# Optimization experiments

Hardware: AMD Instinct MI355X
Metric: run time of the kernel (lower is better)

The kernel has to match this reference:

```python
import jax, jax.numpy as jnp
import numpy as np

S, B, C = 14, 2, 20          # grid size, boxes per cell, classes
LAMBDA_COORD, LAMBDA_NOOBJ = 5.0, 0.5
NCH = 5 * B + C              # 30 channels


def setup_inputs() -> dict:
    key = jax.random.key(0)
    k1, k2, k3 = jax.random.split(key, 3)
    Nb = 4096
    # positive values: loss takes sqrt(w), sqrt(h)
    pred = jax.random.uniform(k1, (Nb, S, S, NCH), dtype=jnp.float32, minval=0.05, maxval=1.0)
    target = jax.random.uniform(k2, (Nb, S, S, NCH), dtype=jnp.float32, minval=0.05, maxval=1.0)
    # binarize conf channels so coord (conf>0) / noobj (conf==0) partition the cells
    objf = (jax.random.uniform(k3, (Nb, S, S)) < 0.3).astype(jnp.float32)
    for b in range(B):
        target = target.at[..., 4 + 5 * b].set(objf)
    return {"pred_tensor": pred, "target_tensor": target}


def _to_xyxy(box):
    # box [..., 5] (or [..., B, 5]): cell-relative x,y and global w,h -> corners
    xy = box[..., :2] / S
    half = 0.5 * box[..., 2:4]
    return jnp.concatenate([xy - half, xy + half], axis=-1)


def reference(pred_tensor, target_tensor):
    pred, target = pred_tensor, target_tensor
    obj = (target[..., 4] > 0).astype(pred.dtype)      # [Nb,S,S]
    noobj = (target[..., 4] == 0).astype(pred.dtype)   # [Nb,S,S]

    pb = pred[..., :5 * B].reshape(pred.shape[:3] + (B, 5))     # [Nb,S,S,B,5]
    tb = target[..., :5 * B].reshape(target.shape[:3] + (B, 5))  # [Nb,S,S,B,5]

    # no-object confidence loss: conf channel of every box slot in noobj cells
    loss_noobj = jnp.sum(noobj[..., None] * (pb[..., 4] - tb[..., 4]) ** 2)

    # IoU of each of B predicted boxes vs the (first) target box of the cell
    pxy = _to_xyxy(pb)                        # [Nb,S,S,B,4]
    txy = _to_xyxy(tb[..., 0, :])[..., None, :]  # [Nb,S,S,1,4]
    lt = jnp.maximum(pxy[..., :2], txy[..., :2])
    rb = jnp.minimum(pxy[..., 2:], txy[..., 2:])
    wh = jnp.clip(rb - lt, 0.0)
    inter = wh[..., 0] * wh[..., 1]           # [Nb,S,S,B]
    area_p = (pxy[..., 2] - pxy[..., 0]) * (pxy[..., 3] - pxy[..., 1])
    area_t = (txy[..., 2] - txy[..., 0]) * (txy[..., 3] - txy[..., 1])
    iou = inter / (area_p + area_t - inter)

    max_iou = jax.lax.stop_gradient(jnp.max(iou, axis=-1))  # torch uses .data (detach)
    r = jnp.argmax(iou, axis=-1)              # responsible box index [Nb,S,S]

    pr = jnp.take_along_axis(pb, r[..., None, None], axis=3)[..., 0, :]  # [Nb,S,S,5]
    tr = jnp.take_along_axis(tb, r[..., None, None], axis=3)[..., 0, :]

    m = obj
    loss_xy = jnp.sum(m[..., None] * (pr[..., :2] - tr[..., :2]) ** 2)
    # guard sqrt in masked-out cells (values there don't matter)
    safe_pwh = jnp.where(m[..., None] > 0, pr[..., 2:4], 1.0)
    safe_twh = jnp.where(m[..., None] > 0, tr[..., 2:4], 1.0)
    loss_wh = jnp.sum(m[..., None] * (jnp.sqrt(safe_pwh) - jnp.sqrt(safe_twh)) ** 2)
    loss_obj = jnp.sum(m * (pr[..., 4] - max_iou) ** 2)
    loss_class = jnp.sum(m[..., None] * (pred[..., 5 * B:] - target[..., 5 * B:]) ** 2)

    loss = LAMBDA_COORD * (loss_xy + loss_wh) + loss_obj + LAMBDA_NOOBJ * loss_noobj + loss_class
    return loss / pred.shape[0]
```

## Files before the change

### kernel.cpp

```cpp
#include <hip/hip_runtime.h>


#define S_GRID 14
#define NB 4096
#define NCELL (NB * S_GRID * S_GRID)
#define NCH 30
#define NBLOCKS (NCELL / 256)

__global__ __launch_bounds__(256) void yolo_loss_partial(
    const float* __restrict__ pred, const float* __restrict__ target,
    float* __restrict__ partial)
{
    const int cell = blockIdx.x * 256 + threadIdx.x;
    float loss = 0.0f;

    {
        float p[NCH], t[NCH];
        const float2* p2 = (const float2*)(pred + (size_t)cell * NCH);
        const float2* t2 = (const float2*)(target + (size_t)cell * NCH);
#pragma unroll
        for (int i = 0; i < NCH / 2; ++i) {
            float2 a = p2[i]; p[2 * i] = a.x; p[2 * i + 1] = a.y;
            float2 b = t2[i]; t[2 * i] = b.x; t[2 * i + 1] = b.y;
        }

        const float t4 = t[4];
        const bool obj = (t4 > 0.0f);

        float dn0 = p[4] - t[4];
        float dn1 = p[9] - t[9];
        float noobj_l = (t4 == 0.0f) ? (dn0 * dn0 + dn1 * dn1) : 0.0f;

        const float invS = 1.0f / 14.0f;
        float tcx = t[0] * invS, tcy = t[1] * invS;
        float tx1 = tcx - 0.5f * t[2], ty1 = tcy - 0.5f * t[3];
        float tx2 = tcx + 0.5f * t[2], ty2 = tcy + 0.5f * t[3];
        float area_t = (tx2 - tx1) * (ty2 - ty1);

        float iou[2];
#pragma unroll
        for (int b = 0; b < 2; ++b) {
            const float* pb = p + 5 * b;
            float cx = pb[0] * invS, cy = pb[1] * invS;
            float x1 = cx - 0.5f * pb[2], y1 = cy - 0.5f * pb[3];
            float x2 = cx + 0.5f * pb[2], y2 = cy + 0.5f * pb[3];
            float lx = fmaxf(x1, tx1), ly = fmaxf(y1, ty1);
            float rx = fminf(x2, tx2), ry = fminf(y2, ty2);
            float wx = fmaxf(rx - lx, 0.0f), wy = fmaxf(ry - ly, 0.0f);
            float inter = wx * wy;
            float area_p = (x2 - x1) * (y2 - y1);
            iou[b] = inter / (area_p + area_t - inter);
        }

        int r = (iou[1] > iou[0]) ? 1 : 0;
        float max_iou = fmaxf(iou[0], iou[1]);

        if (obj) {
            const float* pr = p + 5 * r;
            const float* tr = t + 5 * r;
            float dx = pr[0] - tr[0], dy = pr[1] - tr[1];
            float lxy = dx * dx + dy * dy;
            float dw = sqrtf(pr[2]) - sqrtf(tr[2]);
            float dh = sqrtf(pr[3]) - sqrtf(tr[3]);
            float lwh = dw * dw + dh * dh;
            float dob = pr[4] - max_iou;
            float lob = dob * dob;
            float lcls = 0.0f;
#pragma unroll
            for (int c = 10; c < 30; ++c) {
                float d = p[c] - t[c];
                lcls += d * d;
            }
            loss = 5.0f * (lxy + lwh) + lob + lcls;
        }
        loss += 0.5f * noobj_l;
    }

    float v = loss;
#pragma unroll
    for (int off = 32; off > 0; off >>= 1)
        v += __shfl_down(v, off, 64);

    __shared__ float red[4];
    const int lane = threadIdx.x & 63;
    const int wid = threadIdx.x >> 6;
    if (lane == 0) red[wid] = v;
    __syncthreads();
    if (threadIdx.x == 0)
        partial[blockIdx.x] = red[0] + red[1] + red[2] + red[3];
}

__global__ __launch_bounds__(256) void yolo_loss_finalize(
    const float* __restrict__ partial, float* __restrict__ out)
{
    double s = 0.0;
    for (int i = threadIdx.x; i < NBLOCKS; i += 256)
        s += (double)partial[i];

    __shared__ double sh[256];
    sh[threadIdx.x] = s;
    __syncthreads();
#pragma unroll
    for (int step = 128; step > 0; step >>= 1) {
        if (threadIdx.x < step) sh[threadIdx.x] += sh[threadIdx.x + step];
        __syncthreads();
    }
    if (threadIdx.x == 0)
        out[0] = (float)(sh[0] / (double)NB);
}

extern "C" void kernel_launch(void* const* d_in, const int* in_sizes, int n_in,
                              void* d_out, int out_size, void* d_ws, size_t ws_size,
                              hipStream_t stream) {
    const float* pred = (const float*)d_in[0];
    const float* target = (const float*)d_in[1];
    float* out = (float*)d_out;
    float* partial = (float*)d_ws;

    yolo_loss_partial<<<NBLOCKS, 256, 0, stream>>>(pred, target, partial);
    yolo_loss_finalize<<<1, 256, 0, stream>>>(partial, out);
}
```

Before: 209.2 us.

## Stage pred/target tiles into LDS via coalesced async global-to-LDS copies

Each block now copies its contiguous 256-cell slice of pred and target into shared memory using 16-byte global_load_lds copies. Consecutive threads read consecutive 16-byte chunks, which replaces the per-thread strided 120-byte float2 reads from global memory with fully coalesced traffic. Threads then read their 30 channels from LDS. The cost is 60 KB of LDS per block, which limits occupancy, plus possible LDS bank conflicts from the stride-30 reads. The loss accumulation is also restructured slightly without changing its result.

New measurement: 206.5 us. About the same (-1.3%).

```diff
diff --git a/kernel.cpp b/kernel.cpp
--- a/kernel.cpp
+++ b/kernel.cpp
@@ -5,19 +5,43 @@
 #define NB 4096
 #define NCELL (NB * S_GRID * S_GRID)
 #define NCH 30
-#define NBLOCKS (NCELL / 256)
+#define CELLS_PER_BLOCK 256
+#define NBLOCKS (NCELL / CELLS_PER_BLOCK)
+#define FLOATS_PER_BLOCK (CELLS_PER_BLOCK * NCH)
+
+#define GLOBAL_AS __attribute__((address_space(1)))
+#define LDS_AS    __attribute__((address_space(3)))
+
+__device__ __forceinline__ void async_copy16(const float* g, float* l) {
+    __builtin_amdgcn_global_load_lds((const GLOBAL_AS void*)g, (LDS_AS void*)l,
+                                     16, 0, 0);
+}
 
 __global__ __launch_bounds__(256) void yolo_loss_partial(
     const float* __restrict__ pred, const float* __restrict__ target,
     float* __restrict__ partial)
 {
-    const int cell = blockIdx.x * 256 + threadIdx.x;
-    float loss = 0.0f;
+    __shared__ float ps[FLOATS_PER_BLOCK];
+    __shared__ float ts[FLOATS_PER_BLOCK];
 
+    const int tid = threadIdx.x;
+    const size_t base = (size_t)blockIdx.x * FLOATS_PER_BLOCK;
+
+#pragma unroll
+    for (int r = 0; r < 8; ++r) {
+        int idx = r * 256 + tid;
+        if (idx < FLOATS_PER_BLOCK / 4) {
+            async_copy16(pred + base + (size_t)idx * 4, ps + idx * 4);
+            async_copy16(target + base + (size_t)idx * 4, ts + idx * 4);
+        }
+    }
+    __syncthreads();
+
+    float loss;
     {
         float p[NCH], t[NCH];
-        const float2* p2 = (const float2*)(pred + (size_t)cell * NCH);
-        const float2* t2 = (const float2*)(target + (size_t)cell * NCH);
+        const float2* p2 = (const float2*)(ps + tid * NCH);
+        const float2* t2 = (const float2*)(ts + tid * NCH);
 #pragma unroll
         for (int i = 0; i < NCH / 2; ++i) {
             float2 a = p2[i]; p[2 * i] = a.x; p[2 * i + 1] = a.y;
@@ -55,6 +79,7 @@
         int r = (iou[1] > iou[0]) ? 1 : 0;
         float max_iou = fmaxf(iou[0], iou[1]);
 
+        float obj_l = 0.0f;
         if (obj) {
             const float* pr = p + 5 * r;
             const float* tr = t + 5 * r;
@@ -71,9 +96,9 @@
                 float d = p[c] - t[c];
                 lcls += d * d;
             }
-            loss = 5.0f * (lxy + lwh) + lob + lcls;
+            obj_l = 5.0f * (lxy + lwh) + lob + lcls;
         }
-        loss += 0.5f * noobj_l;
+        loss = obj_l + 0.5f * noobj_l;
     }
 
     float v = loss;
```
